# Kernel tuning notes

Measured on AMD Instinct MI355X. Metric: run time of the kernel, lower is better.

The kernel has to match this reference:

```python
import jax, jax.numpy as jnp
import numpy as np

B, S, D = 32, 4096, 256

def setup_inputs() -> dict:
    key = jax.random.key(0)
    k1, k2, k3 = jax.random.split(key, 3)
    inputs = jax.random.normal(k1, (B, S, D), dtype=jnp.float32)
    W = jax.random.normal(k2, (D, D), dtype=jnp.float32) * 0.05  # 'random_normal' init
    b = jnp.zeros((D,), dtype=jnp.float32)
    V = jax.random.normal(k3, (D, 1), dtype=jnp.float32) * 0.05
    return {"inputs": inputs, "W": W, "b": b, "V": V}

def reference(inputs, W, b, V):
    # score: [B,S,D] = tanh(inputs @ W + b)
    score = jnp.tanh(jnp.einsum('bsd,de->bse', inputs, W) + b)
    # logits: [B,S,1]; softmax over seq axis (axis=1)
    logits = jnp.einsum('bsd,do->bso', score, V)
    attn = jax.nn.softmax(logits, axis=1)            # [B,S,1]
    # weighted sum pooling over seq -> [B,D]
    context = jnp.sum(attn * inputs, axis=1)
    return context
```

## Files before the change

kernel.cpp:

```cpp
#include <hip/hip_runtime.h>
#include <hip/hip_bf16.h>

#define DD 256
#define SS 4096
#define LDK 264

typedef __bf16 bf16x8 __attribute__((ext_vector_type(8)));
typedef float  f32x4  __attribute__((ext_vector_type(4)));

__device__ __forceinline__ float fast_tanh(float x) {
  float e = __expf(2.0f * x);
  return 1.0f - 2.0f / (e + 1.0f);
}

template<int CTRL>
__device__ __forceinline__ float dpp_add(float v) {
  int y = __builtin_amdgcn_update_dpp(0, __float_as_int(v), CTRL, 0xF, 0xF, true);
  return v + __int_as_float(y);
}
__device__ __forceinline__ float row16_sum(float v) {
  v = dpp_add<0xB1>(v);
  v = dpp_add<0x4E>(v);
  v = dpp_add<0x124>(v);
  v = dpp_add<0x128>(v);
  return v;
}

__global__ __launch_bounds__(1024, 1) void fused_kernel(
    const float* __restrict__ X, const float* __restrict__ W,
    const float* __restrict__ bias, const float* __restrict__ V,
    float* __restrict__ Pout, float* __restrict__ Mout, float* __restrict__ Sout)
{
  __shared__ __bf16 Wt[DD * LDK];
  __shared__ float  Pacc[16][DD];
  __shared__ float  Vs[DD];
  __shared__ float  Bs[DD];
  __shared__ float  wred[16];
  __shared__ float  sred[16];

  const int t = threadIdx.x;
  for (int idx = t; idx < DD * DD; idx += 1024) {
    int d = idx >> 8, e = idx & 255;
    Wt[e * LDK + d] = (__bf16)W[idx];
  }
  if (t < DD) { Vs[t] = V[t]; Bs[t] = bias[t]; }
  __syncthreads();

  const int wave = t >> 6, lane = t & 63;
  const int g  = lane >> 4;
  const int lg = lane & 15;
  const size_t rowBase = (size_t)blockIdx.x * 512 + (size_t)wave * 32;

  bf16x8 a[2][8];
  #pragma unroll
  for (int st = 0; st < 2; ++st) {
    const float* xr = X + (rowBase + st * 16 + lg) * DD;
    #pragma unroll
    for (int ks = 0; ks < 8; ++ks) {
      const float4* p = reinterpret_cast<const float4*>(xr + ks * 32 + g * 8);
      float4 f0 = p[0], f1 = p[1];
      bf16x8 fr;
      fr[0] = (__bf16)f0.x; fr[1] = (__bf16)f0.y; fr[2] = (__bf16)f0.z; fr[3] = (__bf16)f0.w;
      fr[4] = (__bf16)f1.x; fr[5] = (__bf16)f1.y; fr[6] = (__bf16)f1.z; fr[7] = (__bf16)f1.w;
      a[st][ks] = fr;
    }
  }

  float sp0[4] = {0.f,0.f,0.f,0.f};
  float sp1[4] = {0.f,0.f,0.f,0.f};
  #pragma unroll 1
  for (int n0 = 0; n0 < 16; ++n0) {
    const int col = n0 * 16 + lg;
    const __bf16* bp = Wt + col * LDK + g * 8;
    f32x4 acc0 = {0.f,0.f,0.f,0.f};
    f32x4 acc1 = {0.f,0.f,0.f,0.f};
    #pragma unroll
    for (int ks = 0; ks < 8; ++ks) {
      bf16x8 bfr = *reinterpret_cast<const bf16x8*>(bp + ks * 32);
      acc0 = __builtin_amdgcn_mfma_f32_16x16x32_bf16(a[0][ks], bfr, acc0, 0, 0, 0);
      acc1 = __builtin_amdgcn_mfma_f32_16x16x32_bf16(a[1][ks], bfr, acc1, 0, 0, 0);
    }
    const float vc = Vs[col], bc = Bs[col];
    #pragma unroll
    for (int r = 0; r < 4; ++r) {
      sp0[r] += fast_tanh(acc0[r] + bc) * vc;
      sp1[r] += fast_tanh(acc1[r] + bc) * vc;
    }
  }

  #pragma unroll
  for (int m = 1; m < 16; m <<= 1) {
    #pragma unroll
    for (int r = 0; r < 4; ++r) {
      sp0[r] += __shfl_xor(sp0[r], m);
      sp1[r] += __shfl_xor(sp1[r], m);
    }
  }
  const int src = ((lg >> 2) << 4) | lg;
  float l0 = 0.f, l1 = 0.f;
  #pragma unroll
  for (int r = 0; r < 4; ++r) {
    float v0 = __shfl(sp0[r], src, 64);
    float v1 = __shfl(sp1[r], src, 64);
    if ((lg & 3) == r) { l0 = v0; l1 = v1; }
  }

  float wm = fmaxf(l0, l1);
  #pragma unroll
  for (int m = 1; m < 16; m <<= 1) wm = fmaxf(wm, __shfl_xor(wm, m));
  if (lane == 0) wred[wave] = wm;
  __syncthreads();
  float M = -1e30f;
  #pragma unroll
  for (int w = 0; w < 16; ++w) M = fmaxf(M, wred[w]);

  const float w0 = __expf(l0 - M);
  const float w1 = __expf(l1 - M);

  float se = w0 + w1;
  #pragma unroll
  for (int m = 1; m < 16; m <<= 1) se += __shfl_xor(se, m);
  if (lane == 0) sred[wave] = se;

  #pragma unroll
  for (int ks = 0; ks < 8; ++ks) {
    float p8[8];
    #pragma unroll
    for (int i = 0; i < 8; ++i)
      p8[i] = w0 * (float)a[0][ks][i] + w1 * (float)a[1][ks][i];
    #pragma unroll
    for (int i = 0; i < 8; ++i) p8[i] = row16_sum(p8[i]);
    if (lg < 2) {
      float4 v = (lg == 0) ? make_float4(p8[0], p8[1], p8[2], p8[3])
                           : make_float4(p8[4], p8[5], p8[6], p8[7]);
      *reinterpret_cast<float4*>(&Pacc[wave][ks * 32 + g * 8 + lg * 4]) = v;
    }
  }
  __syncthreads();

  if (t < DD) {
    float s = 0.f;
    #pragma unroll
    for (int w = 0; w < 16; ++w) s += Pacc[w][t];
    Pout[(size_t)blockIdx.x * DD + t] = s;
  }
  if (t == 0) {
    float ss = 0.f;
    #pragma unroll
    for (int w = 0; w < 16; ++w) ss += sred[w];
    Sout[blockIdx.x] = ss;
    Mout[blockIdx.x] = M;
  }
}

__global__ __launch_bounds__(256) void combine_kernel(
    const float* __restrict__ P, const float* __restrict__ Mb,
    const float* __restrict__ Sb, float* __restrict__ ctx)
{
  const int b = blockIdx.x, t = threadIdx.x;
  float Mg = -1e30f;
  #pragma unroll
  for (int k = 0; k < 8; ++k) Mg = fmaxf(Mg, Mb[b * 8 + k]);
  float denom = 0.f, acc = 0.f;
  #pragma unroll
  for (int k = 0; k < 8; ++k) {
    const float f = __expf(Mb[b * 8 + k] - Mg);
    denom += f * Sb[b * 8 + k];
    acc   += f * P[(size_t)(b * 8 + k) * DD + t];
  }
  ctx[b * DD + t] = acc / denom;
}

extern "C" void kernel_launch(void* const* d_in, const int* in_sizes, int n_in,
                              void* d_out, int out_size, void* d_ws, size_t ws_size,
                              hipStream_t stream) {
  const float* X    = (const float*)d_in[0];
  const float* W    = (const float*)d_in[1];
  const float* bias = (const float*)d_in[2];
  const float* V    = (const float*)d_in[3];
  float* ctx = (float*)d_out;

  float* P = (float*)d_ws;
  float* M = P + 256 * DD;
  float* S = M + 256;

  fused_kernel<<<256, 1024, 0, stream>>>(X, W, bias, V, P, M, S);
  combine_kernel<<<32, 256, 0, stream>>>(P, M, S, ctx);
}
```

Before: 51.96 us.

## Store W in MFMA fragment order in LDS and use DPP row reductions

W is pre-swizzled into LDS in the exact per-lane MFMA B-fragment order, so each lane reads a contiguous 16-byte chunk and avoids the padded transposed layout and its scalar strided LDS writes. Shuffle-based 16-lane reductions for the score sums, max and exp-sum are replaced with DPP row reductions. A waves_per_eu attribute is also added. The new staging loop does strided global reads of W per block, which could cost more than the old coalesced reads.

```diff
diff --git a/kernel.cpp b/kernel.cpp
--- a/kernel.cpp
+++ b/kernel.cpp
@@ -3,7 +3,6 @@
 
 #define DD 256
 #define SS 4096
-#define LDK 264
 
 typedef __bf16 bf16x8 __attribute__((ext_vector_type(8)));
 typedef float  f32x4  __attribute__((ext_vector_type(4)));
@@ -14,24 +13,31 @@
 }
 
 template<int CTRL>
-__device__ __forceinline__ float dpp_add(float v) {
-  int y = __builtin_amdgcn_update_dpp(0, __float_as_int(v), CTRL, 0xF, 0xF, true);
-  return v + __int_as_float(y);
+__device__ __forceinline__ float dpp_mov(float v) {
+  return __int_as_float(__builtin_amdgcn_update_dpp(0, __float_as_int(v), CTRL, 0xF, 0xF, true));
 }
 __device__ __forceinline__ float row16_sum(float v) {
-  v = dpp_add<0xB1>(v);
-  v = dpp_add<0x4E>(v);
-  v = dpp_add<0x124>(v);
-  v = dpp_add<0x128>(v);
+  v += dpp_mov<0xB1>(v);
+  v += dpp_mov<0x4E>(v);
+  v += dpp_mov<0x124>(v);
+  v += dpp_mov<0x128>(v);
+  return v;
+}
+__device__ __forceinline__ float row16_max(float v) {
+  v = fmaxf(v, dpp_mov<0xB1>(v));
+  v = fmaxf(v, dpp_mov<0x4E>(v));
+  v = fmaxf(v, dpp_mov<0x124>(v));
+  v = fmaxf(v, dpp_mov<0x128>(v));
   return v;
 }
 
-__global__ __launch_bounds__(1024, 1) void fused_kernel(
+__global__ __launch_bounds__(1024, 1) __attribute__((amdgpu_waves_per_eu(4)))
+void fused_kernel(
     const float* __restrict__ X, const float* __restrict__ W,
     const float* __restrict__ bias, const float* __restrict__ V,
     float* __restrict__ Pout, float* __restrict__ Mout, float* __restrict__ Sout)
 {
-  __shared__ __bf16 Wt[DD * LDK];
+  __shared__ __bf16 WtF[8192 * 8];
   __shared__ float  Pacc[16][DD];
   __shared__ float  Vs[DD];
   __shared__ float  Bs[DD];
@@ -39,9 +45,17 @@
   __shared__ float  sred[16];
 
   const int t = threadIdx.x;
-  for (int idx = t; idx < DD * DD; idx += 1024) {
-    int d = idx >> 8, e = idx & 255;
-    Wt[e * LDK + d] = (__bf16)W[idx];
+  for (int c = t; c < 8192; c += 1024) {
+    const int lane_c = c & 63;
+    const int ks  = (c >> 6) & 7;
+    const int n0  = c >> 9;
+    const int col = n0 * 16 + (lane_c & 15);
+    const int k0  = ks * 32 + (lane_c >> 4) * 8;
+    const float* wp = W + k0 * DD + col;
+    bf16x8 fr;
+    #pragma unroll
+    for (int i = 0; i < 8; ++i) fr[i] = (__bf16)wp[i * DD];
+    *reinterpret_cast<bf16x8*>(&WtF[(size_t)c * 8]) = fr;
   }
   if (t < DD) { Vs[t] = V[t]; Bs[t] = bias[t]; }
   __syncthreads();
@@ -70,16 +84,16 @@
   float sp1[4] = {0.f,0.f,0.f,0.f};
   #pragma unroll 1
   for (int n0 = 0; n0 < 16; ++n0) {
-    const int col = n0 * 16 + lg;
-    const __bf16* bp = Wt + col * LDK + g * 8;
+    const __bf16* bp = WtF + ((size_t)(n0 * 8) * 64 + lane) * 8;
     f32x4 acc0 = {0.f,0.f,0.f,0.f};
     f32x4 acc1 = {0.f,0.f,0.f,0.f};
     #pragma unroll
     for (int ks = 0; ks < 8; ++ks) {
-      bf16x8 bfr = *reinterpret_cast<const bf16x8*>(bp + ks * 32);
+      bf16x8 bfr = *reinterpret_cast<const bf16x8*>(bp + (size_t)ks * 64 * 8);
       acc0 = __builtin_amdgcn_mfma_f32_16x16x32_bf16(a[0][ks], bfr, acc0, 0, 0, 0);
       acc1 = __builtin_amdgcn_mfma_f32_16x16x32_bf16(a[1][ks], bfr, acc1, 0, 0, 0);
     }
+    const int col = n0 * 16 + lg;
     const float vc = Vs[col], bc = Bs[col];
     #pragma unroll
     for (int r = 0; r < 4; ++r) {
@@ -89,13 +103,8 @@
   }
 
   #pragma unroll
-  for (int m = 1; m < 16; m <<= 1) {
-    #pragma unroll
-    for (int r = 0; r < 4; ++r) {
-      sp0[r] += __shfl_xor(sp0[r], m);
-      sp1[r] += __shfl_xor(sp1[r], m);
-    }
-  }
+  for (int r = 0; r < 4; ++r) { sp0[r] = row16_sum(sp0[r]); sp1[r] = row16_sum(sp1[r]); }
+
   const int src = ((lg >> 2) << 4) | lg;
   float l0 = 0.f, l1 = 0.f;
   #pragma unroll
@@ -105,9 +114,7 @@
     if ((lg & 3) == r) { l0 = v0; l1 = v1; }
   }
 
-  float wm = fmaxf(l0, l1);
-  #pragma unroll
-  for (int m = 1; m < 16; m <<= 1) wm = fmaxf(wm, __shfl_xor(wm, m));
+  float wm = row16_max(fmaxf(l0, l1));
   if (lane == 0) wred[wave] = wm;
   __syncthreads();
   float M = -1e30f;
@@ -117,9 +124,7 @@
   const float w0 = __expf(l0 - M);
   const float w1 = __expf(l1 - M);
 
-  float se = w0 + w1;
-  #pragma unroll
-  for (int m = 1; m < 16; m <<= 1) se += __shfl_xor(se, m);
+  float se = row16_sum(w0 + w1);
   if (lane == 0) sred[wave] = se;
 
   #pragma unroll
```

After: 51.45 us. No clear change (-1.0%).
